# Optimization experiments

Measured on AMD Instinct MI355X. Metric: run time of the kernel, lower is better.

## Reference

```python
import jax, jax.numpy as jnp
import numpy as np

N, E, D, H, DE, L, G = 50000, 800000, 64, 64, 16, 3, 512


def setup_inputs() -> dict:
    key = jax.random.key(0)
    ks = jax.random.split(key, 20)
    s = 0.05  # small init scale for numerical stability
    inp = {
        "x": jax.random.normal(ks[0], (N, D), dtype=jnp.float32),
        "edge_index": jax.random.randint(ks[1], (2, E), 0, N, dtype=jnp.int64),
        "edge_attr": jax.random.normal(ks[2], (E, DE), dtype=jnp.float32),
        "batch_idx": jnp.sort(jax.random.randint(ks[3], (N,), 0, G, dtype=jnp.int64)),
        "mW1": jax.random.normal(ks[4], (L, 2 * H + DE, H), dtype=jnp.float32) * s,
        "mb1": jnp.zeros((L, H), dtype=jnp.float32),
        "mW2": jax.random.normal(ks[5], (L, H, H), dtype=jnp.float32) * s,
        "mb2": jnp.zeros((L, H), dtype=jnp.float32),
        "uW1": jax.random.normal(ks[6], (L, 2 * H, H), dtype=jnp.float32) * s,
        "ub1": jnp.zeros((L, H), dtype=jnp.float32),
        "uW2": jax.random.normal(ks[7], (L, H, H), dtype=jnp.float32) * s,
        "ub2": jnp.zeros((L, H), dtype=jnp.float32),
        "lin1_w": jax.random.normal(ks[8], (H, H), dtype=jnp.float32) * s,
        "lin1_b": jnp.zeros((H,), dtype=jnp.float32),
        "lin2_w": jax.random.normal(ks[9], (H, 1), dtype=jnp.float32) * s,
        "lin2_b": jnp.zeros((1,), dtype=jnp.float32),
        "num_graphs": G,
    }
    return inp


def reference(x, edge_index, edge_attr, batch_idx, mW1, mb1, mW2, mb2,
              uW1, ub1, uW2, ub2, lin1_w, lin1_b, lin2_w, lin2_b, num_graphs):
    src = edge_index[0]  # x_j source nodes
    dst = edge_index[1]  # x_i target nodes (aggregation targets)
    n_nodes = x.shape[0]
    h = x
    for l in range(mW1.shape[0]):  # num_layers (small, fixed)
        # message: MLP(cat[x_i, x_j, edge_attr]) per edge -- [E, 2H+DE]
        m_in = jnp.concatenate([h[dst], h[src], edge_attr], axis=-1)
        m = jax.nn.relu(m_in @ mW1[l] + mb1[l]) @ mW2[l] + mb2[l]
        # aggregate: scatter-add messages into destination nodes -- [N, H]
        agg = jax.ops.segment_sum(m, dst, num_segments=n_nodes)
        # update: MLP(cat[x, aggr_out]), then outer ReLU from the model forward
        u_in = jnp.concatenate([h, agg], axis=-1)
        h = jax.nn.relu(jax.nn.relu(u_in @ uW1[l] + ub1[l]) @ uW2[l] + ub2[l])
    # global mean pool per graph -- [G, H]
    counts = jax.ops.segment_sum(jnp.ones((n_nodes,), h.dtype), batch_idx,
                                 num_segments=num_graphs)
    pooled = jax.ops.segment_sum(h, batch_idx, num_segments=num_graphs)
    pooled = pooled / jnp.maximum(counts, 1.0)[:, None]
    out = jax.nn.relu(pooled @ lin1_w + lin1_b) @ lin2_w + lin2_b  # [G, 1]
    return out
```

## Files before the change

kernel.cpp:

```cpp
#include <hip/hip_runtime.h>

#define H 64

typedef __attribute__((ext_vector_type(8))) short short8;
typedef __attribute__((ext_vector_type(4))) float floatx4;

__device__ __forceinline__ short bf16r(float f) {
    union { float f; unsigned u; } v; v.f = f;
    unsigned r = v.u + 0x7FFFu + ((v.u >> 16) & 1u);
    return (short)(r >> 16);
}

__device__ __forceinline__ float b2f(unsigned short s) {
    union { unsigned u; float f; } v; v.u = ((unsigned)s) << 16; return v.f;
}

__device__ __forceinline__ void pack_one(const float* W, short* out, int K, int KT, int tid)
{
    const int lane = tid & 63;
    const int nt = (tid >> 6) & 3;
    const int lk = tid >> 8;
    const int kt = lk % KT;
    const int lay = lk / KT;
    const int n = nt * 16 + (lane & 15);
    const int kbase = kt * 32 + ((lane >> 4) & 3) * 8;
    short8 v;
#pragma unroll
    for (int j = 0; j < 8; ++j) {
        const int k = kbase + j;
        const float w = (k < K) ? W[((size_t)lay * K + k) * H + n] : 0.f;
        v[j] = bf16r(w);
    }
    *(short8*)(out + (size_t)tid * 8) = v;
}

#define T_MW1 3840
#define T_NW1 3072
#define T_UW2 1536

__global__ void prep_w2u(const float* __restrict__ mW2, const float* __restrict__ uW1,
                         const float* __restrict__ mb2,
                         float* __restrict__ nW1cat, float* __restrict__ c2u)
{
    int g = blockIdx.x * blockDim.x + threadIdx.x;
    if (g < 12288) {
        const int l = g >> 12, rem = g & 4095, a = rem >> 6, j = rem & 63;
        float s = 0.f;
#pragma unroll 8
        for (int c = 0; c < 64; ++c)
            s += mW2[((size_t)l * 64 + a) * 64 + c] * uW1[((size_t)l * 128 + 64 + c) * 64 + j];
        nW1cat[((size_t)l * 128 + 64 + a) * 64 + j] = s;
        return;
    }
    g -= 12288;
    if (g < 12288) {
        const int l = g >> 12, rem = g & 4095;
        nW1cat[(size_t)l * 8192 + rem] = uW1[(size_t)l * 8192 + rem];
        return;
    }
    g -= 12288;
    if (g < 192) {
        const int l = g >> 6, j = g & 63;
        float s = 0.f;
#pragma unroll 8
        for (int c = 0; c < 64; ++c)
            s += mb2[l * 64 + c] * uW1[((size_t)l * 128 + 64 + c) * 64 + j];
        c2u[l * 64 + j] = s;
    }
}

__global__ void prep_all(const float* __restrict__ mW1, const float* __restrict__ nW1cat,
                         const float* __restrict__ uW2, const float* __restrict__ x,
                         short* __restrict__ mW1f, short* __restrict__ nW1f,
                         short* __restrict__ uW2f, short* __restrict__ x16, int n8)
{
    int g = blockIdx.x * blockDim.x + threadIdx.x;
    if (g < T_MW1) { pack_one(mW1, mW1f, 144, 5, g); return; }
    g -= T_MW1;
    if (g < T_NW1) { pack_one(nW1cat, nW1f, 128, 4, g); return; }
    g -= T_NW1;
    if (g < T_UW2) { pack_one(uW2, uW2f, 64, 2, g); return; }
    g -= T_UW2;
    if (g < n8) {
        const float4 a = ((const float4*)x)[2 * g];
        const float4 b = ((const float4*)x)[2 * g + 1];
        short8 v;
        v[0] = bf16r(a.x); v[1] = bf16r(a.y); v[2] = bf16r(a.z); v[3] = bf16r(a.w);
        v[4] = bf16r(b.x); v[5] = bf16r(b.y); v[6] = bf16r(b.z); v[7] = bf16r(b.w);
        ((short8*)x16)[g] = v;
    }
}

__global__ void hist_kernel(const int* __restrict__ edst, int* __restrict__ cnt, int E)
{
    int e = blockIdx.x * blockDim.x + threadIdx.x;
    if (e < E) atomicAdd(&cnt[edst[e]], 1);
}

__global__ void scan_block(const int* __restrict__ cnt, int* __restrict__ offs,
                           int* __restrict__ bsum, int n)
{
    __shared__ int buf[1024];
    const int t = threadIdx.x;
    const int gid = blockIdx.x * 1024 + t;
    const int v = (gid < n) ? cnt[gid] : 0;
    buf[t] = v;
    __syncthreads();
#pragma unroll
    for (int off = 1; off < 1024; off <<= 1) {
        int x = (t >= off) ? buf[t - off] : 0;
        __syncthreads();
        buf[t] += x;
        __syncthreads();
    }
    if (gid < n) offs[gid] = buf[t] - v;
    if (t == 1023) bsum[blockIdx.x] = buf[1023];
}

__global__ void scan_bsum(int* __restrict__ bsum, int nb)
{
    if (threadIdx.x == 0) {
        int acc = 0;
        for (int i = 0; i < nb; ++i) { int v = bsum[i]; bsum[i] = acc; acc += v; }
    }
}

__global__ void add_bsum(int* __restrict__ offs, const int* __restrict__ bsum, int n)
{
    int gid = blockIdx.x * blockDim.x + threadIdx.x;
    if (gid < n) offs[gid] += bsum[gid >> 10];
}

__global__ void build_perm_gather(const int* __restrict__ esrc, const int* __restrict__ edst,
                                  const float* __restrict__ ea, int* __restrict__ offs,
                                  int* __restrict__ src_s, int* __restrict__ dst_s,
                                  short* __restrict__ ea16, int E)
{
    int e = blockIdx.x * blockDim.x + threadIdx.x;
    if (e >= E) return;
    const int d = edst[e];
    const int p = atomicAdd(&offs[d], 1);
    src_s[p] = esrc[e];
    dst_s[p] = d;
    const float4* r = (const float4*)(ea + (size_t)e * 16);
    const float4 a = r[0], b = r[1], c = r[2], d4 = r[3];
    short8 v0, v1;
    v0[0] = bf16r(a.x); v0[1] = bf16r(a.y); v0[2] = bf16r(a.z); v0[3] = bf16r(a.w);
    v0[4] = bf16r(b.x); v0[5] = bf16r(b.y); v0[6] = bf16r(b.z); v0[7] = bf16r(b.w);
    v1[0] = bf16r(c.x); v1[1] = bf16r(c.y); v1[2] = bf16r(c.z); v1[3] = bf16r(c.w);
    v1[4] = bf16r(d4.x); v1[5] = bf16r(d4.y); v1[6] = bf16r(d4.z); v1[7] = bf16r(d4.w);
    short8* o = (short8*)(ea16 + (size_t)p * 16);
    o[0] = v0; o[1] = v1;
}

__global__ __launch_bounds__(256, 5)
void pq_gemm(const short* __restrict__ h16, const short* __restrict__ W1fl,
             short* __restrict__ P16, short* __restrict__ Q16, int N)
{
    const int t = threadIdx.x;
    const int w = t >> 6, l = t & 63, q = l >> 4, m15 = l & 15;
    const int n0 = blockIdx.x * 64;
    const int n = n0 + w * 16 + m15;
    const bool ok = n < N;

    short8 a0 = {0,0,0,0,0,0,0,0}, a1 = a0;
    if (ok) {
        a0 = *(const short8*)(h16 + (size_t)n * H + q * 8);
        a1 = *(const short8*)(h16 + (size_t)n * H + 32 + q * 8);
    }

    floatx4 pa[4] = {{0,0,0,0},{0,0,0,0},{0,0,0,0},{0,0,0,0}};
    floatx4 qa[4] = {{0,0,0,0},{0,0,0,0},{0,0,0,0},{0,0,0,0}};
#pragma unroll
    for (int nt = 0; nt < 4; ++nt) {
        pa[nt] = __builtin_amdgcn_mfma_f32_16x16x32_bf16(a0, *(const short8*)(W1fl + ((0*4+nt)*64 + l)*8), pa[nt], 0,0,0);
        pa[nt] = __builtin_amdgcn_mfma_f32_16x16x32_bf16(a1, *(const short8*)(W1fl + ((1*4+nt)*64 + l)*8), pa[nt], 0,0,0);
        qa[nt] = __builtin_amdgcn_mfma_f32_16x16x32_bf16(a0, *(const short8*)(W1fl + ((2*4+nt)*64 + l)*8), qa[nt], 0,0,0);
        qa[nt] = __builtin_amdgcn_mfma_f32_16x16x32_bf16(a1, *(const short8*)(W1fl + ((3*4+nt)*64 + l)*8), qa[nt], 0,0,0);
    }
#pragma unroll
    for (int nt = 0; nt < 4; ++nt)
#pragma unroll
        for (int r = 0; r < 4; ++r) {
            const int nn = n0 + w * 16 + q * 4 + r;
            if (nn < N) {
                P16[(size_t)nn * H + nt * 16 + m15] = bf16r(pa[nt][r]);
                Q16[(size_t)nn * H + nt * 16 + m15] = bf16r(qa[nt][r]);
            }
        }
}

__global__ __launch_bounds__(256, 5)
void edge_msg_mfma(const short* __restrict__ P16, const short* __restrict__ Q16,
                   const int* __restrict__ src_s, const int* __restrict__ dst_s,
                   const short* __restrict__ ea16,
                   const short* __restrict__ W1cf, const float* __restrict__ b1,
                   float* __restrict__ aggH)
{
    __shared__ float smf[4 * 1056];
    const int t = threadIdx.x;
    const int w = t >> 6, l = t & 63, q = l >> 4, m15 = l & 15;
    const int i = blockIdx.x * 64 + w * 16 + m15;
    const int d = dst_s[i];
    const int s = src_s[i];
    float* C2 = smf + w * 1056;

    int dm[16], sm[16];
#pragma unroll
    for (int mm = 0; mm < 16; ++mm) {
        dm[mm] = __builtin_amdgcn_readlane(d, mm);
        sm[mm] = __builtin_amdgcn_readlane(s, mm);
    }
    float pv[16], qv[16];
#pragma unroll
    for (int mm = 0; mm < 16; ++mm) {
        pv[mm] = b2f((unsigned short)P16[(size_t)dm[mm] * H + l]);
        qv[mm] = b2f((unsigned short)Q16[(size_t)sm[mm] * H + l]);
    }
    const float b1l = b1[l];

    short8 a4 = {0, 0, 0, 0, 0, 0, 0, 0};
    if (q < 2) a4 = *(const short8*)(ea16 + (size_t)i * 16 + q * 8);

    floatx4 r4[4];
#pragma unroll
    for (int nt = 0; nt < 4; ++nt) {
        floatx4 z0 = {0, 0, 0, 0};
        r4[nt] = __builtin_amdgcn_mfma_f32_16x16x32_bf16(a4, *(const short8*)(W1cf + (nt*64 + l)*8), z0, 0,0,0);
    }
#pragma unroll
    for (int nt = 0; nt < 4; ++nt)
#pragma unroll
        for (int r = 0; r < 4; ++r)
            C2[(q * 4 + r) * 66 + nt * 16 + m15] = r4[nt][r];

    float run; int cur;
    {
        run = fmaxf(C2[l] + pv[0] + qv[0] + b1l, 0.f);
        cur = dm[0];
    }
#pragma unroll
    for (int mm = 1; mm < 16; ++mm) {
        const float val = fmaxf(C2[mm * 66 + l] + pv[mm] + qv[mm] + b1l, 0.f);
        if (dm[mm] != cur) {
            atomicAdd(&aggH[(size_t)cur * H + l], run);
            run = val; cur = dm[mm];
        } else {
            run += val;
        }
    }
    atomicAdd(&aggH[(size_t)cur * H + l], run);
}

__global__ __launch_bounds__(256, 5)
void node_update_mfma(const short* __restrict__ h16,
                      const float* __restrict__ aggH,
                      const short* __restrict__ W1f, const float* __restrict__ b1,
                      const short* __restrict__ W2f, const float* __restrict__ b2,
                      const float* __restrict__ c2u, const int* __restrict__ degc,
                      short* __restrict__ h16out,
                      const int* __restrict__ batch,
                      float* __restrict__ pooled, float* __restrict__ counts,
                      int N)
{
    __shared__ char smraw[16896];
    const int t = threadIdx.x;
    const int w = t >> 6, l = t & 63, q = l >> 4, m15 = l & 15;
    const int n0 = blockIdx.x * 64;
    const int n = n0 + w * 16 + m15;
    const bool ok = n < N;

    short* C1 = (short*)(smraw + w * 4224);
    float* C2 = (float*)(smraw + w * 4224);

    short8 a0 = {0,0,0,0,0,0,0,0}, a1 = a0, a2 = a0, a3 = a0;
    if (ok) {
        a0 = *(const short8*)(h16 + (size_t)n * H + q * 8);
        a1 = *(const short8*)(h16 + (size_t)n * H + 32 + q * 8);
        const float4 f0 = *(const float4*)(aggH + (size_t)n * H + q * 8);
        const float4 f1 = *(const float4*)(aggH + (size_t)n * H + q * 8 + 4);
        const float4 f2 = *(const float4*)(aggH + (size_t)n * H + 32 + q * 8);
        const float4 f3 = *(const float4*)(aggH + (size_t)n * H + 32 + q * 8 + 4);
        a2[0] = bf16r(f0.x); a2[1] = bf16r(f0.y); a2[2] = bf16r(f0.z); a2[3] = bf16r(f0.w);
        a2[4] = bf16r(f1.x); a2[5] = bf16r(f1.y); a2[6] = bf16r(f1.z); a2[7] = bf16r(f1.w);
        a3[0] = bf16r(f2.x); a3[1] = bf16r(f2.y); a3[2] = bf16r(f2.z); a3[3] = bf16r(f2.w);
        a3[4] = bf16r(f3.x); a3[5] = bf16r(f3.y); a3[6] = bf16r(f3.z); a3[7] = bf16r(f3.w);
    }

    float b1v[4], b2v[4], c2uv[4];
#pragma unroll
    for (int nt = 0; nt < 4; ++nt) {
        b1v[nt] = b1[nt * 16 + m15];
        b2v[nt] = b2[nt * 16 + m15];
        c2uv[nt] = c2u[nt * 16 + m15];
    }
    float degf[4];
#pragma unroll
    for (int r = 0; r < 4; ++r) {
        const int nn = n0 + w * 16 + q * 4 + r;
        degf[r] = (nn < N) ? (float)degc[nn] : 0.f;
    }

    floatx4 acc[4] = {{0,0,0,0},{0,0,0,0},{0,0,0,0},{0,0,0,0}};
#pragma unroll
    for (int nt = 0; nt < 4; ++nt) {
        acc[nt] = __builtin_amdgcn_mfma_f32_16x16x32_bf16(a0, *(const short8*)(W1f + ((0*4+nt)*64 + l)*8), acc[nt], 0,0,0);
        acc[nt] = __builtin_amdgcn_mfma_f32_16x16x32_bf16(a1, *(const short8*)(W1f + ((1*4+nt)*64 + l)*8), acc[nt], 0,0,0);
        acc[nt] = __builtin_amdgcn_mfma_f32_16x16x32_bf16(a2, *(const short8*)(W1f + ((2*4+nt)*64 + l)*8), acc[nt], 0,0,0);
        acc[nt] = __builtin_amdgcn_mfma_f32_16x16x32_bf16(a3, *(const short8*)(W1f + ((3*4+nt)*64 + l)*8), acc[nt], 0,0,0);
    }

#pragma unroll
    for (int nt = 0; nt < 4; ++nt)
#pragma unroll
        for (int r = 0; r < 4; ++r)
            C1[(q * 4 + r) * 72 + nt * 16 + m15] =
                bf16r(fmaxf(acc[nt][r] + b1v[nt] + degf[r] * c2uv[nt], 0.f));

    const short8 p0 = *(const short8*)(C1 + m15 * 72 + q * 8);
    const short8 p1 = *(const short8*)(C1 + m15 * 72 + 32 + q * 8);

    floatx4 c2[4] = {{0,0,0,0},{0,0,0,0},{0,0,0,0},{0,0,0,0}};
#pragma unroll
    for (int nt = 0; nt < 4; ++nt) {
        c2[nt] = __builtin_amdgcn_mfma_f32_16x16x32_bf16(p0, *(const short8*)(W2f + ((0*4+nt)*64 + l)*8), c2[nt], 0,0,0);
        c2[nt] = __builtin_amdgcn_mfma_f32_16x16x32_bf16(p1, *(const short8*)(W2f + ((1*4+nt)*64 + l)*8), c2[nt], 0,0,0);
    }

    if (!batch) {
#pragma unroll
        for (int nt = 0; nt < 4; ++nt)
#pragma unroll
            for (int r = 0; r < 4; ++r) {
                const int nn = n0 + w * 16 + q * 4 + r;
                if (nn < N)
                    h16out[(size_t)nn * H + nt * 16 + m15] =
                        bf16r(fmaxf(c2[nt][r] + b2v[nt], 0.f));
            }
        return;
    }

#pragma unroll
    for (int nt = 0; nt < 4; ++nt)
#pragma unroll
        for (int r = 0; r < 4; ++r)
            C2[(q * 4 + r) * 66 + nt * 16 + m15] = fmaxf(c2[nt][r] + b2v[nt], 0.f);

    const int bi = ok ? batch[n] : -1;
    int bm[16];
#pragma unroll
    for (int mm = 0; mm < 16; ++mm)
        bm[mm] = __builtin_amdgcn_readlane(bi, mm);
    float v[16];
#pragma unroll
    for (int mm = 0; mm < 16; ++mm) v[mm] = C2[mm * 66 + l];

    float run = v[0];
    int cur = bm[0];
    int len = 1;
#pragma unroll
    for (int mm = 1; mm < 16; ++mm) {
        if (bm[mm] != cur) {
            if (cur >= 0) {
                atomicAdd(&pooled[(size_t)cur * H + l], run);
                if (l == 0) atomicAdd(&counts[cur], (float)len);
            }
            run = v[mm]; cur = bm[mm]; len = 1;
        } else {
            run += v[mm]; ++len;
        }
    }
    if (cur >= 0) {
        atomicAdd(&pooled[(size_t)cur * H + l], run);
        if (l == 0) atomicAdd(&counts[cur], (float)len);
    }
}

__global__ void head_kernel(const float* __restrict__ pooled,
                            const float* __restrict__ counts,
                            const float* __restrict__ lin1w,
                            const float* __restrict__ lin1b,
                            const float* __restrict__ lin2w,
                            const float* __restrict__ lin2b,
                            float* __restrict__ out, int G)
{
    int g = blockIdx.x;
    int j = threadIdx.x;
    __shared__ float p[H];
    float c = fmaxf(counts[g], 1.0f);
    p[j] = pooled[(size_t)g * H + j] / c;
    __syncthreads();

    float accj = lin1b[j];
#pragma unroll
    for (int k = 0; k < H; ++k) accj = fmaf(p[k], lin1w[k * H + j], accj);
    accj = fmaxf(accj, 0.0f) * lin2w[j];
#pragma unroll
    for (int off = 32; off >= 1; off >>= 1) accj += __shfl_down(accj, off);
    if (j == 0) out[g] = accj + lin2b[0];
}

extern "C" void kernel_launch(void* const* d_in, const int* in_sizes, int n_in,
                              void* d_out, int out_size, void* d_ws, size_t ws_size,
                              hipStream_t stream)
{
    const float* x      = (const float*)d_in[0];
    const int*   eidx   = (const int*)d_in[1];
    const float* ea     = (const float*)d_in[2];
    const int*   batch  = (const int*)d_in[3];
    const float* mW1    = (const float*)d_in[4];
    const float* mb1    = (const float*)d_in[5];
    const float* mW2    = (const float*)d_in[6];
    const float* mb2    = (const float*)d_in[7];
    const float* uW1    = (const float*)d_in[8];
    const float* ub1    = (const float*)d_in[9];
    const float* uW2    = (const float*)d_in[10];
    const float* ub2    = (const float*)d_in[11];
    const float* lin1w  = (const float*)d_in[12];
    const float* lin1b  = (const float*)d_in[13];
    const float* lin2w  = (const float*)d_in[14];
    const float* lin2b  = (const float*)d_in[15];

    const int N = in_sizes[0] / H;
    const int E = in_sizes[1] / 2;
    const int G = out_size;

    short* mW1f = (short*)d_ws;
    short* nW1f = mW1f + 30720;
    short* uW2f = nW1f + 24576;
    short* x16  = uW2f + 12288;
    short* h16A = x16  + (size_t)N * H;
    short* h16B = h16A + (size_t)N * H;
    short* ea16 = h16B + (size_t)N * H;
    short* P16  = ea16 + (size_t)E * 16;
    short* Q16  = P16  + (size_t)N * H;
    float* nW1cat = (float*)(Q16 + (size_t)N * H);
    float* c2u    = nW1cat + 3 * 128 * 64;
    char*  pch  = (char*)(c2u + 192);
    int* offs   = (int*)pch;          pch += (size_t)N * 4;
    int* bsum   = (int*)pch;          pch += 256;
    int* src_s  = (int*)pch;          pch += (size_t)E * 4;
    int* dst_s  = (int*)pch;          pch += (size_t)E * 4;
    int*   cnt    = (int*)pch;
    float* agg3   = (float*)(pch + (size_t)N * 4);
    float* pooled = agg3 + (size_t)3 * N * H;
    float* counts = pooled + (size_t)G * H;
    const size_t zero_bytes = (size_t)N * 4 + ((size_t)3 * N * H + (size_t)G * H + G) * 4;

    const int* esrc = eidx;
    const int* edst = eidx + E;

    prep_w2u<<<(24768 + 255) / 256, 256, 0, stream>>>(mW2, uW1, mb2, nW1cat, c2u);
    {
        const int n8 = N * H / 8;
        const int total = T_MW1 + T_NW1 + T_UW2 + n8;
        prep_all<<<(total + 255) / 256, 256, 0, stream>>>(
            mW1, nW1cat, uW2, x, mW1f, nW1f, uW2f, x16, n8);
    }

    hipMemsetAsync(cnt, 0, zero_bytes, stream);

    hist_kernel<<<(E + 255) / 256, 256, 0, stream>>>(edst, cnt, E);
    {
        const int nb = (N + 1023) / 1024;
        scan_block<<<nb, 1024, 0, stream>>>(cnt, offs, bsum, N);
        scan_bsum<<<1, 64, 0, stream>>>(bsum, nb);
        add_bsum<<<(N + 255) / 256, 256, 0, stream>>>(offs, bsum, N);
    }
    build_perm_gather<<<(E + 255) / 256, 256, 0, stream>>>(
        esrc, edst, ea, offs, src_s, dst_s, ea16, E);

    const short* hin = x16;
    short* houts16[3] = {h16A, h16B, nullptr};
    const int nEB = E / 64;
    const int nNB = (N + 63) / 64;

    for (int lyr = 0; lyr < 3; ++lyr) {
        float* agg = agg3 + (size_t)lyr * N * H;
        pq_gemm<<<nNB, 256, 0, stream>>>(
            hin, mW1f + (size_t)lyr * 10240, P16, Q16, N);
        edge_msg_mfma<<<nEB, 256, 0, stream>>>(
            P16, Q16, src_s, dst_s, ea16,
            mW1f + (size_t)lyr * 10240 + 8192,
            mb1 + (size_t)lyr * H,
            agg);
        node_update_mfma<<<nNB, 256, 0, stream>>>(
            hin, agg,
            nW1f + (size_t)lyr * 8192, ub1 + (size_t)lyr * H,
            uW2f + (size_t)lyr * 4096, ub2 + (size_t)lyr * H,
            c2u + (size_t)lyr * 64, cnt,
            houts16[lyr],
            (lyr == 2) ? batch : (const int*)nullptr,
            pooled, counts, N);
        hin = houts16[lyr];
    }

    head_kernel<<<G, H, 0, stream>>>(pooled, counts, lin1w, lin1b, lin2w, lin2b,
                                     (float*)d_out, G);
}
```

Measured before the change: 378.5 us.

## Replace global-atomic counting sort with two-level chunked bucket sort of edges

Edge sorting by destination now runs in two levels. Per-chunk LDS histograms over 64-node buckets are scanned globally, edges and bf16 edge attributes are scattered into buckets, and a second pass sorts each bucket locally in LDS and writes the per-node counts. This is meant to replace the many contended global atomics and fully random scattered writes of the old counting sort with LDS atomics and more localized writes. The cost is an extra read/write pass over the edge data, staged in the agg buffer, which is now zeroed afterwards. It also assumes at most 1024 buckets per chunk histogram.

```diff
diff --git a/kernel.cpp b/kernel.cpp
--- a/kernel.cpp
+++ b/kernel.cpp
@@ -1,6 +1,7 @@
 #include <hip/hip_runtime.h>
 
 #define H 64
+#define CHUNK 8192
 
 typedef __attribute__((ext_vector_type(8))) short short8;
 typedef __attribute__((ext_vector_type(4))) float floatx4;
@@ -91,10 +92,18 @@
     }
 }
 
-__global__ void hist_kernel(const int* __restrict__ edst, int* __restrict__ cnt, int E)
-{
-    int e = blockIdx.x * blockDim.x + threadIdx.x;
-    if (e < E) atomicAdd(&cnt[edst[e]], 1);
+__global__ void chunk_hist(const int* __restrict__ edst, int* __restrict__ ccnt,
+                           int E, int nch, int nbk)
+{
+    __shared__ int lh[1024];
+    const int c = blockIdx.x, t = threadIdx.x;
+    lh[t] = 0;
+    __syncthreads();
+    const int e0 = c * CHUNK, e1 = min(E, e0 + CHUNK);
+    for (int i = e0 + t; i < e1; i += 1024)
+        atomicAdd(&lh[edst[i] >> 6], 1);
+    __syncthreads();
+    if (t < nbk) ccnt[(size_t)t * nch + c] = lh[t];
 }
 
 __global__ void scan_block(const int* __restrict__ cnt, int* __restrict__ offs,
@@ -131,26 +140,68 @@
     if (gid < n) offs[gid] += bsum[gid >> 10];
 }
 
-__global__ void build_perm_gather(const int* __restrict__ esrc, const int* __restrict__ edst,
-                                  const float* __restrict__ ea, int* __restrict__ offs,
-                                  int* __restrict__ src_s, int* __restrict__ dst_s,
-                                  short* __restrict__ ea16, int E)
-{
-    int e = blockIdx.x * blockDim.x + threadIdx.x;
-    if (e >= E) return;
-    const int d = edst[e];
-    const int p = atomicAdd(&offs[d], 1);
-    src_s[p] = esrc[e];
-    dst_s[p] = d;
-    const float4* r = (const float4*)(ea + (size_t)e * 16);
-    const float4 a = r[0], b = r[1], c = r[2], d4 = r[3];
-    short8 v0, v1;
-    v0[0] = bf16r(a.x); v0[1] = bf16r(a.y); v0[2] = bf16r(a.z); v0[3] = bf16r(a.w);
-    v0[4] = bf16r(b.x); v0[5] = bf16r(b.y); v0[6] = bf16r(b.z); v0[7] = bf16r(b.w);
-    v1[0] = bf16r(c.x); v1[1] = bf16r(c.y); v1[2] = bf16r(c.z); v1[3] = bf16r(c.w);
-    v1[4] = bf16r(d4.x); v1[5] = bf16r(d4.y); v1[6] = bf16r(d4.z); v1[7] = bf16r(d4.w);
-    short8* o = (short8*)(ea16 + (size_t)p * 16);
-    o[0] = v0; o[1] = v1;
+__global__ void chunk_scatter(const int* __restrict__ esrc, const int* __restrict__ edst,
+                              const float* __restrict__ ea, const int* __restrict__ cbase,
+                              int2* __restrict__ sd8, short* __restrict__ ear,
+                              int E, int nch)
+{
+    __shared__ int lh[1024];
+    const int c = blockIdx.x, t = threadIdx.x;
+    lh[t] = 0;
+    __syncthreads();
+    const int e0 = c * CHUNK, e1 = min(E, e0 + CHUNK);
+    for (int i = e0 + t; i < e1; i += 1024) {
+        const int d = edst[i];
+        const int b = d >> 6;
+        const int r = atomicAdd(&lh[b], 1);
+        const int p = cbase[(size_t)b * nch + c] + r;
+        sd8[p] = make_int2(esrc[i], d);
+        const float4* rr = (const float4*)(ea + (size_t)i * 16);
+        const float4 a = rr[0], bb = rr[1], cc = rr[2], dd = rr[3];
+        short8 v0, v1;
+        v0[0] = bf16r(a.x);  v0[1] = bf16r(a.y);  v0[2] = bf16r(a.z);  v0[3] = bf16r(a.w);
+        v0[4] = bf16r(bb.x); v0[5] = bf16r(bb.y); v0[6] = bf16r(bb.z); v0[7] = bf16r(bb.w);
+        v1[0] = bf16r(cc.x); v1[1] = bf16r(cc.y); v1[2] = bf16r(cc.z); v1[3] = bf16r(cc.w);
+        v1[4] = bf16r(dd.x); v1[5] = bf16r(dd.y); v1[6] = bf16r(dd.z); v1[7] = bf16r(dd.w);
+        short8* o = (short8*)(ear + (size_t)p * 16);
+        o[0] = v0; o[1] = v1;
+    }
+}
+
+__global__ void bucket_sort(const int2* __restrict__ sd8, const short* __restrict__ ear,
+                            const int* __restrict__ cbase,
+                            int* __restrict__ src_s, int* __restrict__ dst_s,
+                            short* __restrict__ ea16, int* __restrict__ cnt,
+                            int E, int nch, int nbk, int N)
+{
+    __shared__ int c64[64], s64[64];
+    const int b = blockIdx.x, t = threadIdx.x;
+    if (t < 64) c64[t] = 0;
+    __syncthreads();
+    const int es = cbase[(size_t)b * nch];
+    const int ee = (b + 1 < nbk) ? cbase[(size_t)(b + 1) * nch] : E;
+    for (int i = es + t; i < ee; i += 256)
+        atomicAdd(&c64[sd8[i].y & 63], 1);
+    __syncthreads();
+    if (t == 0) {
+        int acc = es;
+        for (int k = 0; k < 64; ++k) { s64[k] = acc; acc += c64[k]; }
+    }
+    __syncthreads();
+    if (t < 64) {
+        const int n = (b << 6) + t;
+        if (n < N) cnt[n] = c64[t];
+    }
+    for (int i = es + t; i < ee; i += 256) {
+        const int2 sd = sd8[i];
+        const int r = atomicAdd(&s64[sd.y & 63], 1);
+        src_s[r] = sd.x;
+        dst_s[r] = sd.y;
+        const short8* si = (const short8*)(ear + (size_t)i * 16);
+        short8 v0 = si[0], v1 = si[1];
+        short8* o = (short8*)(ea16 + (size_t)r * 16);
+        o[0] = v0; o[1] = v1;
+    }
 }
 
 __global__ __launch_bounds__(256, 5)
@@ -424,6 +475,9 @@
     const int N = in_sizes[0] / H;
     const int E = in_sizes[1] / 2;
     const int G = out_size;
+    const int nbk = (N + 63) >> 6;
+    const int nch = (E + CHUNK - 1) / CHUNK;
+    const int Lc  = nbk * nch;
 
     short* mW1f = (short*)d_ws;
     short* nW1f = mW1f + 30720;
@@ -437,15 +491,18 @@
     float* nW1cat = (float*)(Q16 + (size_t)N * H);
     float* c2u    = nW1cat + 3 * 128 * 64;
     char*  pch  = (char*)(c2u + 192);
-    int* offs   = (int*)pch;          pch += (size_t)N * 4;
-    int* bsum   = (int*)pch;          pch += 256;
+    int* ccnt   = (int*)pch;          pch += (size_t)Lc * 4;
+    int* cbase  = (int*)pch;          pch += (size_t)Lc * 4;
+    int* bsum   = (int*)pch;          pch += 1024;
     int* src_s  = (int*)pch;          pch += (size_t)E * 4;
     int* dst_s  = (int*)pch;          pch += (size_t)E * 4;
-    int*   cnt    = (int*)pch;
-    float* agg3   = (float*)(pch + (size_t)N * 4);
+    int* cnt    = (int*)pch;          pch += (size_t)N * 4;
+    float* agg3   = (float*)pch;
     float* pooled = agg3 + (size_t)3 * N * H;
     float* counts = pooled + (size_t)G * H;
-    const size_t zero_bytes = (size_t)N * 4 + ((size_t)3 * N * H + (size_t)G * H + G) * 4;
+    const size_t zero_bytes = ((size_t)3 * N * H + (size_t)G * H + G) * 4;
+    int2*  sd8 = (int2*)agg3;
+    short* ear = (short*)(sd8 + (size_t)E);
 
     const int* esrc = eidx;
     const int* edst = eidx + E;
@@ -458,17 +515,18 @@
             mW1, nW1cat, uW2, x, mW1f, nW1f, uW2f, x16, n8);
     }
 
-    hipMemsetAsync(cnt, 0, zero_bytes, stream);
-
-    hist_kernel<<<(E + 255) / 256, 256, 0, stream>>>(edst, cnt, E);
+    chunk_hist<<<nch, 1024, 0, stream>>>(edst, ccnt, E, nch, nbk);
     {
-        const int nb = (N + 1023) / 1024;
-        scan_block<<<nb, 1024, 0, stream>>>(cnt, offs, bsum, N);
-        scan_bsum<<<1, 64, 0, stream>>>(bsum, nb);
-        add_bsum<<<(N + 255) / 256, 256, 0, stream>>>(offs, bsum, N);
-    }
-    build_perm_gather<<<(E + 255) / 256, 256, 0, stream>>>(
-        esrc, edst, ea, offs, src_s, dst_s, ea16, E);
+        const int nb2 = (Lc + 1023) / 1024;
+        scan_block<<<nb2, 1024, 0, stream>>>(ccnt, cbase, bsum, Lc);
+        scan_bsum<<<1, 64, 0, stream>>>(bsum, nb2);
+        add_bsum<<<(Lc + 255) / 256, 256, 0, stream>>>(cbase, bsum, Lc);
+    }
+    chunk_scatter<<<nch, 1024, 0, stream>>>(esrc, edst, ea, cbase, sd8, ear, E, nch);
+    bucket_sort<<<nbk, 256, 0, stream>>>(sd8, ear, cbase, src_s, dst_s, ea16, cnt,
+                                         E, nch, nbk, N);
+
+    hipMemsetAsync(agg3, 0, zero_bytes, stream);
 
     const short* hin = x16;
     short* houts16[3] = {h16A, h16B, nullptr};
```

After: 407.8 us. +7.7%, slower.

## Fuse next-layer P/Q projection into node update and dedupe P gathers

Applied to the files above, without the earlier changes.

Computes the next layer's P and Q projections inside the node update kernel right after h is produced, using MFMA on the tile already held in shared memory. This removes the separate pq_gemm launches for layers two and three and the re-read of h from global memory. The edge kernel also reloads P only when the destination index changes, which cuts redundant gathers because edges are sorted by destination. The node update launch bound drops from 5 to 4 blocks per CU to make room for the extra accumulators, which may lower occupancy.

```diff
diff --git a/kernel.cpp b/kernel.cpp
--- a/kernel.cpp
+++ b/kernel.cpp
@@ -211,11 +211,20 @@
         dm[mm] = __builtin_amdgcn_readlane(d, mm);
         sm[mm] = __builtin_amdgcn_readlane(s, mm);
     }
-    float pv[16], qv[16];
-#pragma unroll
-    for (int mm = 0; mm < 16; ++mm) {
-        pv[mm] = b2f((unsigned short)P16[(size_t)dm[mm] * H + l]);
+    float qv[16];
+#pragma unroll
+    for (int mm = 0; mm < 16; ++mm)
         qv[mm] = b2f((unsigned short)Q16[(size_t)sm[mm] * H + l]);
+    float pv[16];
+    {
+        float cur = b2f((unsigned short)P16[(size_t)dm[0] * H + l]);
+        pv[0] = cur;
+#pragma unroll
+        for (int mm = 1; mm < 16; ++mm) {
+            if (dm[mm] != dm[mm - 1])
+                cur = b2f((unsigned short)P16[(size_t)dm[mm] * H + l]);
+            pv[mm] = cur;
+        }
     }
     const float b1l = b1[l];
 
@@ -252,13 +261,15 @@
     atomicAdd(&aggH[(size_t)cur * H + l], run);
 }
 
-__global__ __launch_bounds__(256, 5)
+__global__ __launch_bounds__(256, 4)
 void node_update_mfma(const short* __restrict__ h16,
                       const float* __restrict__ aggH,
                       const short* __restrict__ W1f, const float* __restrict__ b1,
                       const short* __restrict__ W2f, const float* __restrict__ b2,
                       const float* __restrict__ c2u, const int* __restrict__ degc,
                       short* __restrict__ h16out,
+                      const short* __restrict__ W1fn,
+                      short* __restrict__ P16o, short* __restrict__ Q16o,
                       const int* __restrict__ batch,
                       float* __restrict__ pooled, float* __restrict__ counts,
                       int N)
@@ -332,11 +343,35 @@
         for (int nt = 0; nt < 4; ++nt)
 #pragma unroll
             for (int r = 0; r < 4; ++r) {
+                const short hv = bf16r(fmaxf(c2[nt][r] + b2v[nt], 0.f));
+                C1[(q * 4 + r) * 72 + nt * 16 + m15] = hv;
                 const int nn = n0 + w * 16 + q * 4 + r;
                 if (nn < N)
-                    h16out[(size_t)nn * H + nt * 16 + m15] =
-                        bf16r(fmaxf(c2[nt][r] + b2v[nt], 0.f));
+                    h16out[(size_t)nn * H + nt * 16 + m15] = hv;
             }
+        if (W1fn) {
+            const short8 h0 = *(const short8*)(C1 + m15 * 72 + q * 8);
+            const short8 h1 = *(const short8*)(C1 + m15 * 72 + 32 + q * 8);
+            floatx4 pa[4] = {{0,0,0,0},{0,0,0,0},{0,0,0,0},{0,0,0,0}};
+            floatx4 qa[4] = {{0,0,0,0},{0,0,0,0},{0,0,0,0},{0,0,0,0}};
+#pragma unroll
+            for (int nt = 0; nt < 4; ++nt) {
+                pa[nt] = __builtin_amdgcn_mfma_f32_16x16x32_bf16(h0, *(const short8*)(W1fn + ((0*4+nt)*64 + l)*8), pa[nt], 0,0,0);
+                pa[nt] = __builtin_amdgcn_mfma_f32_16x16x32_bf16(h1, *(const short8*)(W1fn + ((1*4+nt)*64 + l)*8), pa[nt], 0,0,0);
+                qa[nt] = __builtin_amdgcn_mfma_f32_16x16x32_bf16(h0, *(const short8*)(W1fn + ((2*4+nt)*64 + l)*8), qa[nt], 0,0,0);
+                qa[nt] = __builtin_amdgcn_mfma_f32_16x16x32_bf16(h1, *(const short8*)(W1fn + ((3*4+nt)*64 + l)*8), qa[nt], 0,0,0);
+            }
+#pragma unroll
+            for (int nt = 0; nt < 4; ++nt)
+#pragma unroll
+                for (int r = 0; r < 4; ++r) {
+                    const int nn = n0 + w * 16 + q * 4 + r;
+                    if (nn < N) {
+                        P16o[(size_t)nn * H + nt * 16 + m15] = bf16r(pa[nt][r]);
+                        Q16o[(size_t)nn * H + nt * 16 + m15] = bf16r(qa[nt][r]);
+                    }
+                }
+        }
         return;
     }
 
@@ -475,10 +510,10 @@
     const int nEB = E / 64;
     const int nNB = (N + 63) / 64;
 
+    pq_gemm<<<nNB, 256, 0, stream>>>(x16, mW1f, P16, Q16, N);
+
     for (int lyr = 0; lyr < 3; ++lyr) {
         float* agg = agg3 + (size_t)lyr * N * H;
-        pq_gemm<<<nNB, 256, 0, stream>>>(
-            hin, mW1f + (size_t)lyr * 10240, P16, Q16, N);
         edge_msg_mfma<<<nEB, 256, 0, stream>>>(
             P16, Q16, src_s, dst_s, ea16,
             mW1f + (size_t)lyr * 10240 + 8192,
@@ -490,6 +525,8 @@
             uW2f + (size_t)lyr * 4096, ub2 + (size_t)lyr * H,
             c2u + (size_t)lyr * 64, cnt,
             houts16[lyr],
+            (lyr < 2) ? (mW1f + (size_t)(lyr + 1) * 10240) : (const short*)nullptr,
+            P16, Q16,
             (lyr == 2) ? batch : (const int*)nullptr,
             pooled, counts, N);
         hin = houts16[lyr];
```

Result: slower. 390.0 us (+3.0%).

## Partition edge messages by destination-node windows with LDS accumulation instead of atomics

Applied to the files above, without the earlier changes.

The edge message kernel now launches one wavefront per 16 destination nodes and walks that window's CSR-sorted edge range, accumulating messages into shared memory. Each window writes its results with plain stores, which removes global float atomics and the memset of the three aggregation buffers. Consecutive edges that share a destination also reuse the P gather. The trade-off is load imbalance across windows with uneven degree, a second LDS array that lowers the occupancy target, and a serial loop per wave.

```diff
diff --git a/kernel.cpp b/kernel.cpp
--- a/kernel.cpp
+++ b/kernel.cpp
@@ -190,66 +190,106 @@
         }
 }
 
-__global__ __launch_bounds__(256, 5)
-void edge_msg_mfma(const short* __restrict__ P16, const short* __restrict__ Q16,
-                   const int* __restrict__ src_s, const int* __restrict__ dst_s,
-                   const short* __restrict__ ea16,
-                   const short* __restrict__ W1cf, const float* __restrict__ b1,
-                   float* __restrict__ aggH)
+__global__ __launch_bounds__(256, 4)
+void edge_msg_win(const short* __restrict__ P16, const short* __restrict__ Q16,
+                  const int* __restrict__ src_s, const int* __restrict__ dst_s,
+                  const short* __restrict__ ea16,
+                  const int* __restrict__ offs_end,
+                  const short* __restrict__ W1cf, const float* __restrict__ b1,
+                  float* __restrict__ agg, int N, int E)
 {
     __shared__ float smf[4 * 1056];
+    __shared__ float sacc[4 * 1056];
     const int t = threadIdx.x;
     const int w = t >> 6, l = t & 63, q = l >> 4, m15 = l & 15;
-    const int i = blockIdx.x * 64 + w * 16 + m15;
-    const int d = dst_s[i];
-    const int s = src_s[i];
+    const int g0 = blockIdx.x * 64 + w * 16;
+    if (g0 >= N) return;
     float* C2 = smf + w * 1056;
-
-    int dm[16], sm[16];
-#pragma unroll
-    for (int mm = 0; mm < 16; ++mm) {
-        dm[mm] = __builtin_amdgcn_readlane(d, mm);
-        sm[mm] = __builtin_amdgcn_readlane(s, mm);
-    }
-    float pv[16], qv[16];
-#pragma unroll
-    for (int mm = 0; mm < 16; ++mm) {
-        pv[mm] = b2f((unsigned short)P16[(size_t)dm[mm] * H + l]);
-        qv[mm] = b2f((unsigned short)Q16[(size_t)sm[mm] * H + l]);
-    }
+    float* AC = sacc + w * 1056;
+
+#pragma unroll
+    for (int r = 0; r < 16; ++r) AC[r * 66 + l] = 0.f;
+
+    const int es = (g0 == 0) ? 0 : offs_end[g0 - 1];
+    const int glast = (g0 + 15 < N) ? (g0 + 15) : (N - 1);
+    const int ee = offs_end[glast];
+
     const float b1l = b1[l];
-
-    short8 a4 = {0, 0, 0, 0, 0, 0, 0, 0};
-    if (q < 2) a4 = *(const short8*)(ea16 + (size_t)i * 16 + q * 8);
-
-    floatx4 r4[4];
-#pragma unroll
-    for (int nt = 0; nt < 4; ++nt) {
-        floatx4 z0 = {0, 0, 0, 0};
-        r4[nt] = __builtin_amdgcn_mfma_f32_16x16x32_bf16(a4, *(const short8*)(W1cf + (nt*64 + l)*8), z0, 0,0,0);
-    }
+    short8 wc[4];
 #pragma unroll
     for (int nt = 0; nt < 4; ++nt)
-#pragma unroll
-        for (int r = 0; r < 4; ++r)
-            C2[(q * 4 + r) * 66 + nt * 16 + m15] = r4[nt][r];
-
-    float run; int cur;
-    {
-        run = fmaxf(C2[l] + pv[0] + qv[0] + b1l, 0.f);
-        cur = dm[0];
-    }
-#pragma unroll
-    for (int mm = 1; mm < 16; ++mm) {
-        const float val = fmaxf(C2[mm * 66 + l] + pv[mm] + qv[mm] + b1l, 0.f);
-        if (dm[mm] != cur) {
-            atomicAdd(&aggH[(size_t)cur * H + l], run);
-            run = val; cur = dm[mm];
-        } else {
-            run += val;
-        }
-    }
-    atomicAdd(&aggH[(size_t)cur * H + l], run);
+        wc[nt] = *(const short8*)(W1cf + (nt * 64 + l) * 8);
+
+    int prevd = -1;
+    float pcur = 0.f;
+
+    const int ntl = (ee - es + 15) >> 4;
+    for (int ti = 0; ti < ntl; ++ti) {
+        const int eb = es + ti * 16;
+        const int i0 = eb + m15;
+        const int ic = (i0 < ee) ? i0 : (ee - 1);
+        const int d = dst_s[ic];
+        const int s = src_s[ic];
+
+        int dm[16], sm[16];
+#pragma unroll
+        for (int mm = 0; mm < 16; ++mm) {
+            dm[mm] = __builtin_amdgcn_readlane(d, mm);
+            sm[mm] = __builtin_amdgcn_readlane(s, mm);
+        }
+        float qv[16];
+#pragma unroll
+        for (int mm = 0; mm < 16; ++mm)
+            qv[mm] = b2f((unsigned short)Q16[(size_t)sm[mm] * H + l]);
+        float pv[16];
+#pragma unroll
+        for (int mm = 0; mm < 16; ++mm) {
+            if (dm[mm] != prevd) {
+                pcur = b2f((unsigned short)P16[(size_t)dm[mm] * H + l]);
+                prevd = dm[mm];
+            }
+            pv[mm] = pcur;
+        }
+
+        short8 a4 = {0, 0, 0, 0, 0, 0, 0, 0};
+        if (q < 2) a4 = *(const short8*)(ea16 + (size_t)ic * 16 + q * 8);
+
+        floatx4 r4[4];
+#pragma unroll
+        for (int nt = 0; nt < 4; ++nt) {
+            floatx4 z0 = {0, 0, 0, 0};
+            r4[nt] = __builtin_amdgcn_mfma_f32_16x16x32_bf16(a4, wc[nt], r4[nt] = z0, 0, 0, 0);
+        }
+#pragma unroll
+        for (int nt = 0; nt < 4; ++nt)
+#pragma unroll
+            for (int r = 0; r < 4; ++r)
+                C2[(q * 4 + r) * 66 + nt * 16 + m15] = r4[nt][r];
+
+        float run; int cur;
+        {
+            const float v0 = (eb < ee) ? fmaxf(C2[l] + pv[0] + qv[0] + b1l, 0.f) : 0.f;
+            run = v0; cur = dm[0];
+        }
+#pragma unroll
+        for (int mm = 1; mm < 16; ++mm) {
+            const float val = (eb + mm < ee)
+                ? fmaxf(C2[mm * 66 + l] + pv[mm] + qv[mm] + b1l, 0.f) : 0.f;
+            if (dm[mm] != cur) {
+                AC[(cur - g0) * 66 + l] += run;
+                run = val; cur = dm[mm];
+            } else {
+                run += val;
+            }
+        }
+        AC[(cur - g0) * 66 + l] += run;
+    }
+
+#pragma unroll
+    for (int r = 0; r < 16; ++r) {
+        const int n = g0 + r;
+        if (n < N) agg[(size_t)n * H + l] = AC[r * 66 + l];
+    }
 }
 
 __global__ __launch_bounds__(256, 5)
@@ -441,11 +481,11 @@
     int* bsum   = (int*)pch;          pch += 256;
     int* src_s  = (int*)pch;          pch += (size_t)E * 4;
     int* dst_s  = (int*)pch;          pch += (size_t)E * 4;
+    float* agg3 = (float*)pch;        pch += (size_t)3 * N * H * 4;
     int*   cnt    = (int*)pch;
-    float* agg3   = (float*)(pch + (size_t)N * 4);
-    float* pooled = agg3 + (size_t)3 * N * H;
+    float* pooled = (float*)(pch + (size_t)N * 4);
     float* counts = pooled + (size_t)G * H;
-    const size_t zero_bytes = (size_t)N * 4 + ((size_t)3 * N * H + (size_t)G * H + G) * 4;
+    const size_t zero_bytes = (size_t)N * 4 + ((size_t)G * H + G) * 4;
 
     const int* esrc = eidx;
     const int* edst = eidx + E;
@@ -472,18 +512,17 @@
 
     const short* hin = x16;
     short* houts16[3] = {h16A, h16B, nullptr};
-    const int nEB = E / 64;
     const int nNB = (N + 63) / 64;
 
     for (int lyr = 0; lyr < 3; ++lyr) {
         float* agg = agg3 + (size_t)lyr * N * H;
         pq_gemm<<<nNB, 256, 0, stream>>>(
             hin, mW1f + (size_t)lyr * 10240, P16, Q16, N);
-        edge_msg_mfma<<<nEB, 256, 0, stream>>>(
-            P16, Q16, src_s, dst_s, ea16,
+        edge_msg_win<<<nNB, 256, 0, stream>>>(
+            P16, Q16, src_s, dst_s, ea16, offs,
             mW1f + (size_t)lyr * 10240 + 8192,
             mb1 + (size_t)lyr * H,
-            agg);
+            agg, N, E);
         node_update_mfma<<<nNB, 256, 0, stream>>>(
             hin, agg,
             nW1f + (size_t)lyr * 8192, ub1 + (size_t)lyr * H,
```

Result: slower. 487.8 us (+28.9%).
